# Performance work log

Measured on AMD Instinct MI355X. Metric: run time of the kernel, lower is better.

Reference implementation:

```python
import jax, jax.numpy as jnp
import numpy as np

d_model = 512


def setup_inputs() -> dict:
    key = jax.random.key(0)
    k1, k2, k3, k4 = jax.random.split(key, 4)
    B, T, d_k = 8, 2048, 64
    scale = 1.0 / np.sqrt(d_model)
    x = jax.random.normal(k1, (B, T, d_model), dtype=jnp.float32)
    Wk = jax.random.normal(k2, (d_model, d_k), dtype=jnp.float32) * scale
    Wq = jax.random.normal(k3, (d_model, d_k), dtype=jnp.float32) * scale
    Wv = jax.random.normal(k4, (d_model, d_k), dtype=jnp.float32) * scale
    return {"x": x, "Wk": Wk, "Wq": Wq, "Wv": Wv}


def reference(x, Wk, Wq, Wv):
    # x: [B,T,C]; W*: [C,d_k]  (torch Linear weight is [d_k,C]; we store transposed)
    k = jnp.einsum('btc,cd->btd', x, Wk)
    q = jnp.einsum('btc,cd->btd', x, Wq)
    v = jnp.einsum('btc,cd->btd', x, Wv)
    d_k = k.shape[-1]
    scores = jnp.einsum('bqd,bkd->bqk', q, k) / jnp.sqrt(jnp.float32(d_k))
    attn = jax.nn.softmax(scores, axis=-1)  # [B,T,T]
    return jnp.einsum('bqk,bkd->bqd', attn, v)
```

## Files before the change

### kernel.cpp

```cpp
#include <hip/hip_runtime.h>
#include <hip/hip_bf16.h>
#include <stdint.h>


typedef short bf16x8 __attribute__((ext_vector_type(8)));
typedef float f32x4 __attribute__((ext_vector_type(4)));

#define MFMA_BF16 __builtin_amdgcn_mfma_f32_16x16x32_bf16

__device__ __forceinline__ unsigned int pk2(float a, float b) {
    __hip_bfloat162 h = __float22bfloat162_rn(float2{a, b});
    union { __hip_bfloat162 h; unsigned int u; } r; r.h = h;
    return r.u;
}

__device__ __forceinline__ uint2 pack4_bf16(float a, float b, float c, float d) {
    uint2 r; r.x = pk2(a, b); r.y = pk2(c, d); return r;
}

__device__ __forceinline__ bf16x8 cvt8(f32x4 a, f32x4 b) {
    union { bf16x8 v; unsigned int u[4]; } r;
    r.u[0] = pk2(a[0], a[1]); r.u[1] = pk2(a[2], a[3]);
    r.u[2] = pk2(b[0], b[1]); r.u[3] = pk2(b[2], b[3]);
    return r.v;
}

__device__ __forceinline__ unsigned short bf1(float a) {
    __hip_bfloat16 h = __float2bfloat16(a);
    union { __hip_bfloat16 h; unsigned short u; } r; r.h = h;
    return r.u;
}

__global__ void prep_kernel(const float* __restrict__ x,
                            const float* __restrict__ Wq,
                            const float* __restrict__ Wk,
                            const float* __restrict__ Wv,
                            unsigned short* __restrict__ xb2,
                            unsigned short* __restrict__ wt2)
{
    if (blockIdx.x < 48) {
        int id = blockIdx.x * 256 + threadIdx.x;
        int c    = id & 15;
        int quad = (id >> 4) & 3;
        int ks   = (id >> 6) & 15;
        int mt   = (id >> 10) & 3;
        int w    = id >> 12;
        const float* src = (w == 0) ? Wq : ((w == 1) ? Wk : Wv);
        const int n  = mt * 16 + c;
        const int k0 = ks * 32 + quad * 8;
        unsigned short* dst = wt2 + (size_t)id * 8;
        #pragma unroll
        for (int j = 0; j < 8; j++)
            dst[j] = bf1(src[(size_t)(k0 + j) * 64 + n]);
        return;
    }
    int i = (blockIdx.x - 48) * 256 + threadIdx.x;
    int tok    = i >> 6;
    int dblock = i & 63;
    f32x4 a = *(const f32x4*)(x + (size_t)i * 8);
    f32x4 b = *(const f32x4*)(x + (size_t)i * 8 + 4);
    int tt = tok >> 4, c = tok & 15;
    int ks = dblock >> 2, quad = dblock & 3;
    size_t chunk = ((size_t)(tt * 16 + ks) * 4 + quad) * 16 + c;
    *(bf16x8*)(xb2 + chunk * 8) = cvt8(a, b);
}

__global__ __launch_bounds__(256, 1) void proj_kernel(
    const unsigned short* __restrict__ xb2, const unsigned short* __restrict__ wt2,
    unsigned short* __restrict__ qg, unsigned short* __restrict__ kg2,
    unsigned short* __restrict__ vg2)
{
    const int lane = threadIdx.x & 63;
    const int c    = lane & 15;
    const int quad = lane >> 4;
    const int wave = threadIdx.x >> 6;
    const int gw   = blockIdx.x * 4 + wave;
    const int w    = gw % 3;
    const int tt   = gw / 3;
    const int t0   = tt * 16;

    f32x4 acc[4];
    #pragma unroll
    for (int i = 0; i < 4; i++) acc[i] = f32x4{0.f, 0.f, 0.f, 0.f};

    const unsigned short* xbase = xb2 + ((size_t)tt * 16 * 64 + lane) * 8;
    const unsigned short* wbase = wt2 + ((size_t)w * 4 * 16 * 64 + lane) * 8;

    #pragma unroll 4
    for (int ks = 0; ks < 16; ks++) {
        bf16x8 xf = *(const bf16x8*)(xbase + (size_t)ks * 64 * 8);
        #pragma unroll
        for (int mt = 0; mt < 4; mt++) {
            bf16x8 wa = *(const bf16x8*)(wbase + ((size_t)mt * 16 + ks) * 64 * 8);
            acc[mt] = MFMA_BF16(wa, xf, acc[mt], 0, 0, 0);
        }
    }

    const int b  = t0 >> 11;
    const int tb = t0 & 2047;

    if (w == 0) {
        unsigned short* base = qg + (size_t)(t0 + c) * 64;
        #pragma unroll
        for (int mt = 0; mt < 4; mt++)
            *(uint2*)(base + mt * 16 + quad * 4) =
                pack4_bf16(acc[mt][0], acc[mt][1], acc[mt][2], acc[mt][3]);
    } else if (w == 1) {
        const int g = tb >> 4;
        #pragma unroll
        for (int mt = 0; mt < 4; mt++) {
            const int h  = mt >> 1;
            const int qk = (mt & 1) * 2 + (quad >> 1);
            size_t chunk = (size_t)b * 16384 + ((size_t)(g * 2 + h) * 4 + qk) * 16 + c;
            *(uint2*)(kg2 + chunk * 8 + (quad & 1) * 4) =
                pack4_bf16(acc[mt][0], acc[mt][1], acc[mt][2], acc[mt][3]);
        }
    } else {
        const int tk = tb + c;
        const int s  = tk >> 5;
        const int qv = (tk >> 3) & 3;
        const int j  = tk & 7;
        #pragma unroll
        for (int mt = 0; mt < 4; mt++) {
            size_t chunk = (size_t)b * 16384 + ((size_t)(s * 4 + mt) * 4 + qv) * 16 + quad * 4;
            unsigned short* dst = vg2 + chunk * 8 + j;
            dst[0]  = bf1(acc[mt][0]);
            dst[8]  = bf1(acc[mt][1]);
            dst[16] = bf1(acc[mt][2]);
            dst[24] = bf1(acc[mt][3]);
        }
    }
}

__global__ __launch_bounds__(256, 1) void attn_kernel(
    const unsigned short* __restrict__ qg, const unsigned short* __restrict__ kg2,
    const unsigned short* __restrict__ vg2, float* __restrict__ out)
{
    __shared__ unsigned short pt[4][2][16 * 136];
    __shared__ float obuf[4][2][16][68];
    __shared__ float lbuf[4][2][16];

    const int lane = threadIdx.x & 63;
    const int wave = threadIdx.x >> 6;
    const int c    = lane & 15;
    const int quad = lane >> 4;
    const int b    = blockIdx.x & 7;
    const int g    = blockIdx.x >> 3;
    const int tb   = b * 2048 + g * 32;

    unsigned short* ptw = &pt[wave][0][0];
    const unsigned short* kbase = kg2 + ((size_t)b * 16384 + lane) * 8;
    const unsigned short* vbase = vg2 + ((size_t)b * 16384 + lane) * 8;

    bf16x8 qa0 = *(const bf16x8*)(qg + (size_t)(tb + c) * 64 + quad * 8);
    bf16x8 qa1 = *(const bf16x8*)(qg + (size_t)(tb + c) * 64 + 32 + quad * 8);
    bf16x8 qc0 = *(const bf16x8*)(qg + (size_t)(tb + 16 + c) * 64 + quad * 8);
    bf16x8 qc1 = *(const bf16x8*)(qg + (size_t)(tb + 16 + c) * 64 + 32 + quad * 8);

    f32x4 oa0 = {0,0,0,0}, oa1 = {0,0,0,0}, oa2 = {0,0,0,0}, oa3 = {0,0,0,0};
    f32x4 ob0 = {0,0,0,0}, ob1 = {0,0,0,0}, ob2 = {0,0,0,0}, ob3 = {0,0,0,0};
    f32x4 laccA = {0,0,0,0}, laccB = {0,0,0,0};
    const float cexp = 0.18033688011112042f;

    for (int kt = wave * 4; kt < wave * 4 + 4; kt++) {
        const int key0 = kt * 128;
        const int g0   = key0 >> 4;
        const int s0   = key0 >> 5;

        f32x4 stA[8], stB[8];
        const f32x4 z = {0,0,0,0};
        #pragma unroll
        for (int mt = 0; mt < 8; mt++) {
            bf16x8 k0 = *(const bf16x8*)(kbase + (size_t)((g0 + mt) * 2    ) * 64 * 8);
            bf16x8 k1 = *(const bf16x8*)(kbase + (size_t)((g0 + mt) * 2 + 1) * 64 * 8);
            stA[mt] = MFMA_BF16(k0, qa0, z, 0, 0, 0);
            stA[mt] = MFMA_BF16(k1, qa1, stA[mt], 0, 0, 0);
            stB[mt] = MFMA_BF16(k0, qc0, z, 0, 0, 0);
            stB[mt] = MFMA_BF16(k1, qc1, stB[mt], 0, 0, 0);
        }

        bf16x8 va[2][4];
        #pragma unroll
        for (int mt = 0; mt < 4; mt++) {
            va[0][mt] = *(const bf16x8*)(vbase + (size_t)((s0    ) * 4 + mt) * 64 * 8);
            va[1][mt] = *(const bf16x8*)(vbase + (size_t)((s0 + 1) * 4 + mt) * 64 * 8);
        }

        asm volatile("" ::: "memory");
        #pragma unroll
        for (int mt = 0; mt < 8; mt++) {
            float p0 = __builtin_amdgcn_exp2f(stA[mt][0] * cexp);
            float p1 = __builtin_amdgcn_exp2f(stA[mt][1] * cexp);
            float p2 = __builtin_amdgcn_exp2f(stA[mt][2] * cexp);
            float p3 = __builtin_amdgcn_exp2f(stA[mt][3] * cexp);
            laccA[0] += p0; laccA[1] += p1; laccA[2] += p2; laccA[3] += p3;
            *(uint2*)(ptw + c * 136 + mt * 16 + quad * 4) = pack4_bf16(p0, p1, p2, p3);
        }
        #pragma unroll
        for (int mt = 0; mt < 8; mt++) {
            float p0 = __builtin_amdgcn_exp2f(stB[mt][0] * cexp);
            float p1 = __builtin_amdgcn_exp2f(stB[mt][1] * cexp);
            float p2 = __builtin_amdgcn_exp2f(stB[mt][2] * cexp);
            float p3 = __builtin_amdgcn_exp2f(stB[mt][3] * cexp);
            laccB[0] += p0; laccB[1] += p1; laccB[2] += p2; laccB[3] += p3;
            *(uint2*)(ptw + 2176 + c * 136 + mt * 16 + quad * 4) = pack4_bf16(p0, p1, p2, p3);
        }
        asm volatile("" ::: "memory");

        #pragma unroll
        for (int ks = 0; ks < 4; ks++) {
            bf16x8 pbA = *(const bf16x8*)(ptw + c * 136 + ks * 32 + quad * 8);
            bf16x8 pbB = *(const bf16x8*)(ptw + 2176 + c * 136 + ks * 32 + quad * 8);
            bf16x8 v0 = va[ks & 1][0], v1 = va[ks & 1][1];
            bf16x8 v2 = va[ks & 1][2], v3 = va[ks & 1][3];
            if (ks < 2) {
                #pragma unroll
                for (int mt = 0; mt < 4; mt++)
                    va[ks & 1][mt] =
                        *(const bf16x8*)(vbase + (size_t)((s0 + ks + 2) * 4 + mt) * 64 * 8);
            }
            oa0 = MFMA_BF16(v0, pbA, oa0, 0, 0, 0);
            oa1 = MFMA_BF16(v1, pbA, oa1, 0, 0, 0);
            oa2 = MFMA_BF16(v2, pbA, oa2, 0, 0, 0);
            oa3 = MFMA_BF16(v3, pbA, oa3, 0, 0, 0);
            ob0 = MFMA_BF16(v0, pbB, ob0, 0, 0, 0);
            ob1 = MFMA_BF16(v1, pbB, ob1, 0, 0, 0);
            ob2 = MFMA_BF16(v2, pbB, ob2, 0, 0, 0);
            ob3 = MFMA_BF16(v3, pbB, ob3, 0, 0, 0);
        }
        asm volatile("" ::: "memory");
    }

    float lA = (laccA[0] + laccA[1]) + (laccA[2] + laccA[3]);
    lA += __shfl_xor(lA, 16);
    lA += __shfl_xor(lA, 32);
    float lB = (laccB[0] + laccB[1]) + (laccB[2] + laccB[3]);
    lB += __shfl_xor(lB, 16);
    lB += __shfl_xor(lB, 32);

    *(f32x4*)&obuf[wave][0][c][ 0 + quad * 4] = oa0;
    *(f32x4*)&obuf[wave][0][c][16 + quad * 4] = oa1;
    *(f32x4*)&obuf[wave][0][c][32 + quad * 4] = oa2;
    *(f32x4*)&obuf[wave][0][c][48 + quad * 4] = oa3;
    *(f32x4*)&obuf[wave][1][c][ 0 + quad * 4] = ob0;
    *(f32x4*)&obuf[wave][1][c][16 + quad * 4] = ob1;
    *(f32x4*)&obuf[wave][1][c][32 + quad * 4] = ob2;
    *(f32x4*)&obuf[wave][1][c][48 + quad * 4] = ob3;
    if (quad == 0) { lbuf[wave][0][c] = lA; lbuf[wave][1][c] = lB; }
    __syncthreads();

    const int tid = threadIdx.x;
    const int row = tid >> 3;
    const int d0  = (tid & 7) * 8;
    const int qt  = row >> 4;
    const int r   = row & 15;
    const float L = (lbuf[0][qt][r] + lbuf[1][qt][r]) +
                    (lbuf[2][qt][r] + lbuf[3][qt][r]);
    const float rl = 1.f / L;
    f32x4 Oa = {0,0,0,0}, Ob = {0,0,0,0};
    #pragma unroll
    for (int w = 0; w < 4; w++) {
        f32x4 a = *(const f32x4*)&obuf[w][qt][r][d0];
        f32x4 bfr = *(const f32x4*)&obuf[w][qt][r][d0 + 4];
        Oa[0] += a[0]; Oa[1] += a[1]; Oa[2] += a[2]; Oa[3] += a[3];
        Ob[0] += bfr[0]; Ob[1] += bfr[1]; Ob[2] += bfr[2]; Ob[3] += bfr[3];
    }
    Oa[0] *= rl; Oa[1] *= rl; Oa[2] *= rl; Oa[3] *= rl;
    Ob[0] *= rl; Ob[1] *= rl; Ob[2] *= rl; Ob[3] *= rl;
    float* op = out + (size_t)(tb + row) * 64 + d0;
    *(f32x4*)op       = Oa;
    *(f32x4*)(op + 4) = Ob;
}

extern "C" void kernel_launch(void* const* d_in, const int* in_sizes, int n_in,
                              void* d_out, int out_size, void* d_ws, size_t ws_size,
                              hipStream_t stream)
{
    const float* x  = (const float*)d_in[0];
    const float* Wk = (const float*)d_in[1];
    const float* Wq = (const float*)d_in[2];
    const float* Wv = (const float*)d_in[3];
    float* out = (float*)d_out;

    char* ws = (char*)d_ws;
    unsigned short* qg  = (unsigned short*)(ws);
    unsigned short* kg2 = (unsigned short*)(ws + (2u << 20));
    unsigned short* vg2 = (unsigned short*)(ws + (4u << 20));
    unsigned short* wt2 = (unsigned short*)(ws + (6u << 20));
    unsigned short* xb2 = (unsigned short*)(ws + (7u << 20));

    hipLaunchKernelGGL(prep_kernel, dim3(4144), dim3(256), 0, stream,
                       x, Wq, Wk, Wv, xb2, wt2);
    hipLaunchKernelGGL(proj_kernel, dim3(768),  dim3(256), 0, stream,
                       xb2, wt2, qg, kg2, vg2);
    hipLaunchKernelGGL(attn_kernel, dim3(512),  dim3(256), 0, stream,
                       qg, kg2, vg2, out);
}
```

Baseline: 110.2 us.

## Reuse weight fragments across two token tiles in projection; hoist V loads

The projection kernel now runs 3 waves per block, one each for Q, K and V, and each wave computes two 16-token tiles. Every loaded weight fragment therefore feeds two MFMAs, halving weight traffic per output, and the launch drops to 512 blocks of 192 threads. In the attention kernel the V fragment loads move ahead of the QK MFMAs so their latency can overlap the score computation. The cost is more live registers and fewer, smaller blocks in the projection kernel.

```diff
diff --git a/kernel.cpp b/kernel.cpp
--- a/kernel.cpp
+++ b/kernel.cpp
@@ -65,7 +65,7 @@
     *(bf16x8*)(xb2 + chunk * 8) = cvt8(a, b);
 }
 
-__global__ __launch_bounds__(256, 1) void proj_kernel(
+__global__ __launch_bounds__(192, 1) void proj_kernel(
     const unsigned short* __restrict__ xb2, const unsigned short* __restrict__ wt2,
     unsigned short* __restrict__ qg, unsigned short* __restrict__ kg2,
     unsigned short* __restrict__ vg2)
@@ -73,61 +73,67 @@
     const int lane = threadIdx.x & 63;
     const int c    = lane & 15;
     const int quad = lane >> 4;
-    const int wave = threadIdx.x >> 6;
-    const int gw   = blockIdx.x * 4 + wave;
-    const int w    = gw % 3;
-    const int tt   = gw / 3;
-    const int t0   = tt * 16;
-
-    f32x4 acc[4];
+    const int w    = threadIdx.x >> 6;
+    const int tp   = blockIdx.x;
+
+    f32x4 acc[2][4];
     #pragma unroll
-    for (int i = 0; i < 4; i++) acc[i] = f32x4{0.f, 0.f, 0.f, 0.f};
-
-    const unsigned short* xbase = xb2 + ((size_t)tt * 16 * 64 + lane) * 8;
-    const unsigned short* wbase = wt2 + ((size_t)w * 4 * 16 * 64 + lane) * 8;
+    for (int i = 0; i < 2; i++)
+        #pragma unroll
+        for (int mt = 0; mt < 4; mt++) acc[i][mt] = f32x4{0.f, 0.f, 0.f, 0.f};
+
+    const unsigned short* xbase0 = xb2 + ((size_t)(tp * 2    ) * 1024 + lane) * 8;
+    const unsigned short* xbase1 = xb2 + ((size_t)(tp * 2 + 1) * 1024 + lane) * 8;
+    const unsigned short* wbase  = wt2 + ((size_t)w * 4096 + lane) * 8;
 
     #pragma unroll 4
     for (int ks = 0; ks < 16; ks++) {
-        bf16x8 xf = *(const bf16x8*)(xbase + (size_t)ks * 64 * 8);
+        bf16x8 xf0 = *(const bf16x8*)(xbase0 + (size_t)ks * 512);
+        bf16x8 xf1 = *(const bf16x8*)(xbase1 + (size_t)ks * 512);
         #pragma unroll
         for (int mt = 0; mt < 4; mt++) {
-            bf16x8 wa = *(const bf16x8*)(wbase + ((size_t)mt * 16 + ks) * 64 * 8);
-            acc[mt] = MFMA_BF16(wa, xf, acc[mt], 0, 0, 0);
-        }
-    }
-
-    const int b  = t0 >> 11;
-    const int tb = t0 & 2047;
-
-    if (w == 0) {
-        unsigned short* base = qg + (size_t)(t0 + c) * 64;
-        #pragma unroll
-        for (int mt = 0; mt < 4; mt++)
-            *(uint2*)(base + mt * 16 + quad * 4) =
-                pack4_bf16(acc[mt][0], acc[mt][1], acc[mt][2], acc[mt][3]);
-    } else if (w == 1) {
-        const int g = tb >> 4;
-        #pragma unroll
-        for (int mt = 0; mt < 4; mt++) {
-            const int h  = mt >> 1;
-            const int qk = (mt & 1) * 2 + (quad >> 1);
-            size_t chunk = (size_t)b * 16384 + ((size_t)(g * 2 + h) * 4 + qk) * 16 + c;
-            *(uint2*)(kg2 + chunk * 8 + (quad & 1) * 4) =
-                pack4_bf16(acc[mt][0], acc[mt][1], acc[mt][2], acc[mt][3]);
-        }
-    } else {
-        const int tk = tb + c;
-        const int s  = tk >> 5;
-        const int qv = (tk >> 3) & 3;
-        const int j  = tk & 7;
-        #pragma unroll
-        for (int mt = 0; mt < 4; mt++) {
-            size_t chunk = (size_t)b * 16384 + ((size_t)(s * 4 + mt) * 4 + qv) * 16 + quad * 4;
-            unsigned short* dst = vg2 + chunk * 8 + j;
-            dst[0]  = bf1(acc[mt][0]);
-            dst[8]  = bf1(acc[mt][1]);
-            dst[16] = bf1(acc[mt][2]);
-            dst[24] = bf1(acc[mt][3]);
+            bf16x8 wa = *(const bf16x8*)(wbase + ((size_t)mt * 16 + ks) * 512);
+            acc[0][mt] = MFMA_BF16(wa, xf0, acc[0][mt], 0, 0, 0);
+            acc[1][mt] = MFMA_BF16(wa, xf1, acc[1][mt], 0, 0, 0);
+        }
+    }
+
+    #pragma unroll
+    for (int i = 0; i < 2; i++) {
+        const int t0 = (tp * 2 + i) * 16;
+        const int b  = t0 >> 11;
+        const int tb = t0 & 2047;
+
+        if (w == 0) {
+            unsigned short* base = qg + (size_t)(t0 + c) * 64;
+            #pragma unroll
+            for (int mt = 0; mt < 4; mt++)
+                *(uint2*)(base + mt * 16 + quad * 4) =
+                    pack4_bf16(acc[i][mt][0], acc[i][mt][1], acc[i][mt][2], acc[i][mt][3]);
+        } else if (w == 1) {
+            const int g = tb >> 4;
+            #pragma unroll
+            for (int mt = 0; mt < 4; mt++) {
+                const int h  = mt >> 1;
+                const int qk = (mt & 1) * 2 + (quad >> 1);
+                size_t chunk = (size_t)b * 16384 + ((size_t)(g * 2 + h) * 4 + qk) * 16 + c;
+                *(uint2*)(kg2 + chunk * 8 + (quad & 1) * 4) =
+                    pack4_bf16(acc[i][mt][0], acc[i][mt][1], acc[i][mt][2], acc[i][mt][3]);
+            }
+        } else {
+            const int tk = tb + c;
+            const int s  = tk >> 5;
+            const int qv = (tk >> 3) & 3;
+            const int j  = tk & 7;
+            #pragma unroll
+            for (int mt = 0; mt < 4; mt++) {
+                size_t chunk = (size_t)b * 16384 + ((size_t)(s * 4 + mt) * 4 + qv) * 16 + quad * 4;
+                unsigned short* dst = vg2 + chunk * 8 + j;
+                dst[0]  = bf1(acc[i][mt][0]);
+                dst[8]  = bf1(acc[i][mt][1]);
+                dst[16] = bf1(acc[i][mt][2]);
+                dst[24] = bf1(acc[i][mt][3]);
+            }
         }
     }
 }
@@ -167,6 +173,13 @@
         const int g0   = key0 >> 4;
         const int s0   = key0 >> 5;
 
+        bf16x8 va[2][4];
+        #pragma unroll
+        for (int mt = 0; mt < 4; mt++) {
+            va[0][mt] = *(const bf16x8*)(vbase + (size_t)((s0    ) * 4 + mt) * 64 * 8);
+            va[1][mt] = *(const bf16x8*)(vbase + (size_t)((s0 + 1) * 4 + mt) * 64 * 8);
+        }
+
         f32x4 stA[8], stB[8];
         const f32x4 z = {0,0,0,0};
         #pragma unroll
@@ -177,13 +190,6 @@
             stA[mt] = MFMA_BF16(k1, qa1, stA[mt], 0, 0, 0);
             stB[mt] = MFMA_BF16(k0, qc0, z, 0, 0, 0);
             stB[mt] = MFMA_BF16(k1, qc1, stB[mt], 0, 0, 0);
-        }
-
-        bf16x8 va[2][4];
-        #pragma unroll
-        for (int mt = 0; mt < 4; mt++) {
-            va[0][mt] = *(const bf16x8*)(vbase + (size_t)((s0    ) * 4 + mt) * 64 * 8);
-            va[1][mt] = *(const bf16x8*)(vbase + (size_t)((s0 + 1) * 4 + mt) * 64 * 8);
         }
 
         asm volatile("" ::: "memory");
@@ -291,7 +297,7 @@
 
     hipLaunchKernelGGL(prep_kernel, dim3(4144), dim3(256), 0, stream,
                        x, Wq, Wk, Wv, xb2, wt2);
-    hipLaunchKernelGGL(proj_kernel, dim3(768),  dim3(256), 0, stream,
+    hipLaunchKernelGGL(proj_kernel, dim3(512),  dim3(192), 0, stream,
                        xb2, wt2, qg, kg2, vg2);
     hipLaunchKernelGGL(attn_kernel, dim3(512),  dim3(256), 0, stream,
                        qg, kg2, vg2, out);
```

Result: slower. 113.2 us (+2.7%).
